# Performance work log

Measured on AMD Instinct MI355X. Metric: run time of the kernel, lower is better.

Reference implementation:

```python
import jax, jax.numpy as jnp
import numpy as np

SIGMA = 1.0
RADIUS = int(4.0 * SIGMA + 0.5)  # scipy/skimage truncate=4.0

_t = np.arange(-RADIUS, RADIUS + 1, dtype=np.float32)
_w = np.exp(-0.5 * (_t / SIGMA) ** 2)
KERNEL = jnp.asarray(_w / _w.sum())  # [2*RADIUS+1]


def _blur_axis(x, axis):
    """1D Gaussian filter along `axis` with 'nearest' (edge) boundary."""
    pads = [(0, 0)] * x.ndim
    pads[axis] = (RADIUS, RADIUS)
    xp = jnp.pad(x, pads, mode='edge')
    n = x.shape[axis]
    out = KERNEL[0] * jax.lax.slice_in_dim(xp, 0, n, axis=axis)
    for k in range(1, 2 * RADIUS + 1):
        out = out + KERNEL[k] * jax.lax.slice_in_dim(xp, k, k + n, axis=axis)
    return out


def gaussian_blur(x):
    # skimage.filters.gaussian on each [T, F] sample: blur over both axes
    x = _blur_axis(x, axis=1)  # time axis
    x = _blur_axis(x, axis=2)  # feature axis
    return x


def lstm_last_hidden(x, W_ih, W_hh, b_ih, b_hh):
    B, T, F = x.shape
    H = W_hh.shape[1]
    # precompute input projections for all timesteps: [B, T, 4H]
    xg = jnp.einsum('btf,gf->btg', x, W_ih) + b_ih + b_hh
    xg = jnp.transpose(xg, (1, 0, 2))  # [T, B, 4H]

    def step(carry, xt):
        h, c = carry
        g = xt + h @ W_hh.T  # [B, 4H]
        i, f, gg, o = jnp.split(g, 4, axis=-1)  # torch gate order i,f,g,o
        i = jax.nn.sigmoid(i)
        f = jax.nn.sigmoid(f)
        gg = jnp.tanh(gg)
        o = jax.nn.sigmoid(o)
        c = f * c + i * gg
        h = o * jnp.tanh(c)
        return (h, c), None

    h0 = jnp.zeros((B, H), dtype=x.dtype)
    c0 = jnp.zeros((B, H), dtype=x.dtype)
    (h_last, _), _ = jax.lax.scan(step, (h0, c0), xg)
    return h_last  # [B, H]


def setup_inputs() -> dict:
    key = jax.random.key(0)
    ks = jax.random.split(key, 7)
    B, T, F, H, O = 64, 1024, 256, 1024, 256
    s_ih = 1.0 / np.sqrt(F)
    s_hh = 1.0 / np.sqrt(H)
    return {
        'x': jax.random.uniform(ks[0], (B, T, F), dtype=jnp.float32),
        'W_ih': jax.random.normal(ks[1], (4 * H, F), dtype=jnp.float32) * s_ih,
        'W_hh': jax.random.normal(ks[2], (4 * H, H), dtype=jnp.float32) * s_hh,
        'b_ih': jax.random.normal(ks[3], (4 * H,), dtype=jnp.float32) * s_hh,
        'b_hh': jax.random.normal(ks[4], (4 * H,), dtype=jnp.float32) * s_hh,
        'W_fc': jax.random.normal(ks[5], (O, H), dtype=jnp.float32) * s_hh,
        'b_fc': jax.random.normal(ks[6], (O,), dtype=jnp.float32) * s_hh,
    }


def reference(x, W_ih, W_hh, b_ih, b_hh, W_fc, b_fc):
    xb = gaussian_blur(x)
    h_last = lstm_last_hidden(xb, W_ih, W_hh, b_ih, b_hh)
    return h_last @ W_fc.T + b_fc  # [B, O]
```

## Files before the change

### kernel.cpp

```cpp
#include <hip/hip_runtime.h>

typedef __bf16 bf16x8 __attribute__((ext_vector_type(8)));
typedef float f32x4 __attribute__((ext_vector_type(4)));

#define T_STEPS 1024
#define H_SZ    1024
#define F_IN    256
#define NGROUP  4
#define NB      16
#define WPG     64

__device__ __forceinline__ unsigned short f2bf(float f) {
    union { float f; unsigned u; } v; v.f = f;
    unsigned r = v.u + 0x7fffu + ((v.u >> 16) & 1u);
    return (unsigned short)(r >> 16);
}

__device__ __forceinline__ float fsigmoid(float x) {
    return 1.0f / (1.0f + __expf(-x));
}
__device__ __forceinline__ float ftanh(float x) {
    return 1.0f - 2.0f / (__expf(2.0f * x) + 1.0f);
}

__device__ __forceinline__ int redidx(int h, int b) {
    return ((4 * h + b) & 31) + 32 * ((h >> 3) * 4 + (b >> 2));
}

__global__ __launch_bounds__(256) void blur_kernel(
    const float* __restrict__ x, unsigned short* __restrict__ xb)
{
    __shared__ float tb[64][256];
    const float kk[9] = {
        0.000133831f, 0.0044318617f, 0.0539911273f, 0.2419714457f,
        0.3989434694f,
        0.2419714457f, 0.0539911273f, 0.0044318617f, 0.000133831f };

    const int b     = blockIdx.x >> 4;
    const int chunk = blockIdx.x & 15;
    const int t0    = chunk * 64;
    const int f     = threadIdx.x;
    const float* xbase = x + (size_t)b * T_STEPS * F_IN;

    for (int r = 0; r < 64; r++) {
        int t = t0 + r;
        float acc = 0.0f;
        #pragma unroll
        for (int d = 0; d < 9; d++) {
            int ts = t + d - 4;
            ts = min(max(ts, 0), T_STEPS - 1);
            acc += kk[d] * xbase[ts * F_IN + f];
        }
        tb[r][f] = acc;
    }
    __syncthreads();
    for (int r = 0; r < 64; r++) {
        float acc = 0.0f;
        #pragma unroll
        for (int d = 0; d < 9; d++) {
            int fs = f + d - 4;
            fs = min(max(fs, 0), F_IN - 1);
            acc += kk[d] * tb[r][fs];
        }
        xb[((size_t)b * T_STEPS + t0 + r) * F_IN + f] = f2bf(acc);
    }
}

__global__ __launch_bounds__(256, 1) void lstm_persist(
    const unsigned short* __restrict__ xb,
    const float* __restrict__ Whh,
    const float* __restrict__ Wih,
    const float* __restrict__ bih,
    const float* __restrict__ bhh,
    unsigned short* __restrict__ hbuf,
    unsigned int* __restrict__ arrive)
{
    const int wg   = blockIdx.x;
    const int grp  = wg >> 6;
    const int w    = wg & 63;
    const int tid  = threadIdx.x;
    const int q    = tid >> 6;
    const int lane = tid & 63;
    const int lrow = lane & 15;
    const int lq   = lane >> 4;

    __shared__ float red[4][4][256];

    bf16x8 wa[8][4];
    bf16x8 wx[2][4];
    const int row_lo = w * 16 + lrow;
    #pragma unroll
    for (int kt = 0; kt < 8; kt++) {
        const int kofs = q * 256 + kt * 32 + lq * 8;
        #pragma unroll
        for (int g = 0; g < 4; g++) {
            const float* src = Whh + (size_t)(g * H_SZ + row_lo) * H_SZ + kofs;
            union { bf16x8 v; unsigned short s[8]; } u;
            #pragma unroll
            for (int j = 0; j < 8; j++) u.s[j] = f2bf(src[j]);
            wa[kt][g] = u.v;
        }
    }
    #pragma unroll
    for (int kt = 0; kt < 2; kt++) {
        const int kofs = q * 64 + kt * 32 + lq * 8;
        #pragma unroll
        for (int g = 0; g < 4; g++) {
            const float* src = Wih + (size_t)(g * H_SZ + row_lo) * F_IN + kofs;
            union { bf16x8 v; unsigned short s[8]; } u;
            #pragma unroll
            for (int j = 0; j < 8; j++) u.s[j] = f2bf(src[j]);
            wx[kt][g] = u.v;
        }
    }

    const int uhid = tid & 15;
    const int ub   = tid >> 4;
    float bias[4];
    #pragma unroll
    for (int g = 0; g < 4; g++) {
        int r = g * H_SZ + w * 16 + uhid;
        bias[g] = bih[r] + bhh[r];
    }
    float c_reg = 0.0f;

    const int b_abs_l = grp * NB + lrow;
    const unsigned short* xrow_base =
        xb + ((size_t)b_abs_l * T_STEPS) * F_IN + q * 64 + lq * 8;
    unsigned short* hdst =
        hbuf + (size_t)(grp * NB + ub) * H_SZ + w * 16 + uhid;

    int wofs[4];
    #pragma unroll
    for (int e = 0; e < 4; e++) wofs[e] = redidx(lq * 4 + e, lrow);
    const int rofs = redidx(uhid, ub);

    for (int t = 0; t < T_STEPS; t++) {
        const unsigned short* xrow = xrow_base + (size_t)t * F_IN;
        bf16x8 xf0 = *reinterpret_cast<const bf16x8*>(xrow);
        bf16x8 xf1 = *reinterpret_cast<const bf16x8*>(xrow + 32);

        const unsigned short* hprev =
            hbuf + ((size_t)((t & 1) ^ 1) * 64 + b_abs_l) * H_SZ
                 + q * 256 + lq * 8;
        bf16x8 hf0, hf1, hf2, hf3, hf4, hf5, hf6, hf7;
        asm volatile(
            "global_load_dwordx4 %0, %8, off sc0 sc1\n\t"
            "global_load_dwordx4 %1, %8, off offset:64 sc0 sc1\n\t"
            "global_load_dwordx4 %2, %8, off offset:128 sc0 sc1\n\t"
            "global_load_dwordx4 %3, %8, off offset:192 sc0 sc1\n\t"
            "global_load_dwordx4 %4, %8, off offset:256 sc0 sc1\n\t"
            "global_load_dwordx4 %5, %8, off offset:320 sc0 sc1\n\t"
            "global_load_dwordx4 %6, %8, off offset:384 sc0 sc1\n\t"
            "global_load_dwordx4 %7, %8, off offset:448 sc0 sc1\n\t"
            "s_waitcnt vmcnt(0)"
            : "=&v"(hf0), "=&v"(hf1), "=&v"(hf2), "=&v"(hf3),
              "=&v"(hf4), "=&v"(hf5), "=&v"(hf6), "=&v"(hf7)
            : "v"(hprev)
            : "memory");
        bf16x8 hfa[8] = { hf0, hf1, hf2, hf3, hf4, hf5, hf6, hf7 };

        f32x4 acc[4];
        #pragma unroll
        for (int g = 0; g < 4; g++) acc[g] = (f32x4){0.f, 0.f, 0.f, 0.f};
        #pragma unroll
        for (int kt = 0; kt < 8; kt++)
            #pragma unroll
            for (int g = 0; g < 4; g++)
                acc[g] = __builtin_amdgcn_mfma_f32_16x16x32_bf16(
                    wa[kt][g], hfa[kt], acc[g], 0, 0, 0);
        acc[0] = __builtin_amdgcn_mfma_f32_16x16x32_bf16(wx[0][0], xf0, acc[0], 0, 0, 0);
        acc[1] = __builtin_amdgcn_mfma_f32_16x16x32_bf16(wx[0][1], xf0, acc[1], 0, 0, 0);
        acc[2] = __builtin_amdgcn_mfma_f32_16x16x32_bf16(wx[0][2], xf0, acc[2], 0, 0, 0);
        acc[3] = __builtin_amdgcn_mfma_f32_16x16x32_bf16(wx[0][3], xf0, acc[3], 0, 0, 0);
        acc[0] = __builtin_amdgcn_mfma_f32_16x16x32_bf16(wx[1][0], xf1, acc[0], 0, 0, 0);
        acc[1] = __builtin_amdgcn_mfma_f32_16x16x32_bf16(wx[1][1], xf1, acc[1], 0, 0, 0);
        acc[2] = __builtin_amdgcn_mfma_f32_16x16x32_bf16(wx[1][2], xf1, acc[2], 0, 0, 0);
        acc[3] = __builtin_amdgcn_mfma_f32_16x16x32_bf16(wx[1][3], xf1, acc[3], 0, 0, 0);

        #pragma unroll
        for (int g = 0; g < 4; g++)
            #pragma unroll
            for (int e = 0; e < 4; e++)
                red[q][g][wofs[e]] = acc[g][e];
        __syncthreads();

        float gv[4];
        #pragma unroll
        for (int g = 0; g < 4; g++) {
            float s = bias[g];
            #pragma unroll
            for (int qq = 0; qq < 4; qq++)
                s += red[qq][g][rofs];
            gv[g] = s;
        }
        float ig = fsigmoid(gv[0]);
        float fg = fsigmoid(gv[1]);
        float gg = ftanh(gv[2]);
        float og = fsigmoid(gv[3]);
        c_reg = fg * c_reg + ig * gg;
        float hv = og * ftanh(c_reg);

        unsigned short hb = f2bf(hv);
        unsigned short* dst = hdst + (size_t)(t & 1) * 64 * H_SZ;
        asm volatile(
            "global_store_short %0, %1, off sc0 sc1\n\t"
            "s_waitcnt vmcnt(0)"
            :: "v"(dst), "v"(hb)
            : "memory");
        __syncthreads();

        unsigned int* bar = arrive + (((size_t)grp * T_STEPS + t) << 6);
        if (tid == 0)
            asm volatile("global_atomic_add %0, %1, off"
                         :: "v"(bar + (w & 3) * 16), "v"(1u) : "memory");
        if (tid < 4) {
            const unsigned int* p = bar + tid * 16;
            unsigned v; int spins = 0;
            for (;;) {
                asm volatile("global_load_dword %0, %1, off sc0 sc1\n\t"
                             "s_waitcnt vmcnt(0)"
                             : "=v"(v) : "v"(p) : "memory");
                if (v >= 16u) break;
                if (++spins > (1 << 20)) break;
            }
        }
        __syncthreads();
    }
}

__global__ __launch_bounds__(256) void final_fc(
    const unsigned short* __restrict__ hbuf,
    const float* __restrict__ Wfc, const float* __restrict__ bfc,
    float* __restrict__ out)
{
    __shared__ float hs[H_SZ];
    const int b = blockIdx.x;
    const unsigned short* hrow = hbuf + (size_t)64 * H_SZ + (size_t)b * H_SZ;
    for (int k = threadIdx.x; k < H_SZ; k += 256) {
        union { unsigned u; float f; } cv;
        cv.u = ((unsigned)hrow[k]) << 16;
        hs[k] = cv.f;
    }
    __syncthreads();
    const int o = threadIdx.x;
    const float4* wr = reinterpret_cast<const float4*>(Wfc + (size_t)o * H_SZ);
    float acc = bfc[o];
    for (int k4 = 0; k4 < H_SZ / 4; k4++) {
        float4 wv = wr[k4];
        acc += hs[k4 * 4 + 0] * wv.x + hs[k4 * 4 + 1] * wv.y
             + hs[k4 * 4 + 2] * wv.z + hs[k4 * 4 + 3] * wv.w;
    }
    out[(size_t)b * 256 + o] = acc;
}

extern "C" void kernel_launch(void* const* d_in, const int* in_sizes, int n_in,
                              void* d_out, int out_size, void* d_ws,
                              size_t ws_size, hipStream_t stream)
{
    (void)in_sizes; (void)n_in; (void)out_size; (void)ws_size;
    const float* x   = (const float*)d_in[0];
    const float* Wih = (const float*)d_in[1];
    const float* Whh = (const float*)d_in[2];
    const float* bih = (const float*)d_in[3];
    const float* bhh = (const float*)d_in[4];
    const float* Wfc = (const float*)d_in[5];
    const float* bfc = (const float*)d_in[6];
    float* out = (float*)d_out;

    char* ws = (char*)d_ws;
    unsigned short* xblur = (unsigned short*)ws;
    unsigned short* hbuf  = (unsigned short*)(ws + 33554432);
    unsigned int*   arrv  = (unsigned int*)(ws + 33554432 + 262144);

    hipMemsetAsync(hbuf, 0, 262144 + 1048576, stream);

    blur_kernel<<<dim3(1024), dim3(256), 0, stream>>>(x, xblur);

    void* kargs[] = { (void*)&xblur, (void*)&Whh, (void*)&Wih,
                      (void*)&bih, (void*)&bhh, (void*)&hbuf, (void*)&arrv };
    hipLaunchCooperativeKernel((void*)lstm_persist, dim3(256), dim3(256),
                               kargs, 0, stream);

    final_fc<<<dim3(64), dim3(256), 0, stream>>>(hbuf, Wfc, bfc, out);
}
```

Baseline: 3.762 ms.

## Interleave two half-batch LSTM groups per workgroup to hide barrier latency

Each workgroup now handles two 8-sample sub-groups (A and B) of its 16-sample slice and alternates between them within each timestep. Each sub-group has its own barrier counters, so the wait on one sub-group's grid barrier overlaps with computing the other sub-group's step. The next h loads are issued before the store and wait, so they overlap too. The MFMA tiles are now half-filled, which doubles matrix work per sample. The spin loop now bails out permanently after a short timeout, which risks silently wrong results if a wait is unusually long.

Result: slower. 5.582 ms (+48.4%).

```diff
diff --git a/kernel.cpp b/kernel.cpp
--- a/kernel.cpp
+++ b/kernel.cpp
@@ -6,9 +6,10 @@
 #define T_STEPS 1024
 #define H_SZ    1024
 #define F_IN    256
-#define NGROUP  4
-#define NB      16
+#define NGR     8
+#define NB      8
 #define WPG     64
+#define SPIN_MAX (1 << 15)
 
 __device__ __forceinline__ unsigned short f2bf(float f) {
     union { float f; unsigned u; } v; v.f = f;
@@ -25,6 +26,24 @@
 
 __device__ __forceinline__ int redidx(int h, int b) {
     return ((4 * h + b) & 31) + 32 * ((h >> 3) * 4 + (b >> 2));
+}
+
+__device__ __forceinline__ void issue_h8(const unsigned short* p,
+    bf16x8& h0, bf16x8& h1, bf16x8& h2, bf16x8& h3,
+    bf16x8& h4, bf16x8& h5, bf16x8& h6, bf16x8& h7)
+{
+    asm volatile(
+        "global_load_dwordx4 %0, %8, off sc0 sc1\n\t"
+        "global_load_dwordx4 %1, %8, off offset:64 sc0 sc1\n\t"
+        "global_load_dwordx4 %2, %8, off offset:128 sc0 sc1\n\t"
+        "global_load_dwordx4 %3, %8, off offset:192 sc0 sc1\n\t"
+        "global_load_dwordx4 %4, %8, off offset:256 sc0 sc1\n\t"
+        "global_load_dwordx4 %5, %8, off offset:320 sc0 sc1\n\t"
+        "global_load_dwordx4 %6, %8, off offset:384 sc0 sc1\n\t"
+        "global_load_dwordx4 %7, %8, off offset:448 sc0 sc1"
+        : "=&v"(h0), "=&v"(h1), "=&v"(h2), "=&v"(h3),
+          "=&v"(h4), "=&v"(h5), "=&v"(h6), "=&v"(h7)
+        : "v"(p) : "memory");
 }
 
 __global__ __launch_bounds__(256) void blur_kernel(
@@ -76,13 +95,16 @@
     unsigned int* __restrict__ arrive)
 {
     const int wg   = blockIdx.x;
-    const int grp  = wg >> 6;
+    const int pid  = wg >> 6;
     const int w    = wg & 63;
     const int tid  = threadIdx.x;
     const int q    = tid >> 6;
     const int lane = tid & 63;
     const int lrow = lane & 15;
     const int lq   = lane >> 4;
+    const int bl   = lrow & 7;
+    const int gA   = pid * 2;
+    const int gB   = pid * 2 + 1;
 
     __shared__ float red[4][4][256];
 
@@ -115,117 +137,186 @@
     }
 
     const int uhid = tid & 15;
-    const int ub   = tid >> 4;
+    const int ub   = (tid >> 4) & 7;
     float bias[4];
     #pragma unroll
     for (int g = 0; g < 4; g++) {
         int r = g * H_SZ + w * 16 + uhid;
         bias[g] = bih[r] + bhh[r];
     }
-    float c_reg = 0.0f;
-
-    const int b_abs_l = grp * NB + lrow;
-    const unsigned short* xrow_base =
-        xb + ((size_t)b_abs_l * T_STEPS) * F_IN + q * 64 + lq * 8;
-    unsigned short* hdst =
-        hbuf + (size_t)(grp * NB + ub) * H_SZ + w * 16 + uhid;
+    float cA = 0.0f, cB = 0.0f;
+
+    const int bA = pid * 16 + bl;
+    const unsigned short* xbaseA =
+        xb + ((size_t)bA * T_STEPS) * F_IN + q * 64 + lq * 8;
+    const unsigned short* xbaseB = xbaseA + (size_t)8 * T_STEPS * F_IN;
+    unsigned short* hdstA =
+        hbuf + (size_t)(pid * 16 + ub) * H_SZ + w * 16 + uhid;
+    unsigned short* hdstB = hdstA + (size_t)8 * H_SZ;
+    const unsigned short* hsrcA =
+        hbuf + (size_t)bA * H_SZ + q * 256 + lq * 8;
+    const unsigned short* hsrcB = hsrcA + (size_t)8 * H_SZ;
 
     int wofs[4];
     #pragma unroll
-    for (int e = 0; e < 4; e++) wofs[e] = redidx(lq * 4 + e, lrow);
+    for (int e = 0; e < 4; e++) wofs[e] = redidx(lq * 4 + e, bl);
     const int rofs = redidx(uhid, ub);
 
+    bf16x8 hf0, hf1, hf2, hf3, hf4, hf5, hf6, hf7;
+    int bail = 0;
+
+    issue_h8(hsrcA + (size_t)64 * H_SZ, hf0, hf1, hf2, hf3, hf4, hf5, hf6, hf7);
+
     for (int t = 0; t < T_STEPS; t++) {
-        const unsigned short* xrow = xrow_base + (size_t)t * F_IN;
-        bf16x8 xf0 = *reinterpret_cast<const bf16x8*>(xrow);
-        bf16x8 xf1 = *reinterpret_cast<const bf16x8*>(xrow + 32);
-
-        const unsigned short* hprev =
-            hbuf + ((size_t)((t & 1) ^ 1) * 64 + b_abs_l) * H_SZ
-                 + q * 256 + lq * 8;
-        bf16x8 hf0, hf1, hf2, hf3, hf4, hf5, hf6, hf7;
-        asm volatile(
-            "global_load_dwordx4 %0, %8, off sc0 sc1\n\t"
-            "global_load_dwordx4 %1, %8, off offset:64 sc0 sc1\n\t"
-            "global_load_dwordx4 %2, %8, off offset:128 sc0 sc1\n\t"
-            "global_load_dwordx4 %3, %8, off offset:192 sc0 sc1\n\t"
-            "global_load_dwordx4 %4, %8, off offset:256 sc0 sc1\n\t"
-            "global_load_dwordx4 %5, %8, off offset:320 sc0 sc1\n\t"
-            "global_load_dwordx4 %6, %8, off offset:384 sc0 sc1\n\t"
-            "global_load_dwordx4 %7, %8, off offset:448 sc0 sc1\n\t"
-            "s_waitcnt vmcnt(0)"
-            : "=&v"(hf0), "=&v"(hf1), "=&v"(hf2), "=&v"(hf3),
-              "=&v"(hf4), "=&v"(hf5), "=&v"(hf6), "=&v"(hf7)
-            : "v"(hprev)
-            : "memory");
-        bf16x8 hfa[8] = { hf0, hf1, hf2, hf3, hf4, hf5, hf6, hf7 };
+        const size_t par  = (size_t)(t & 1) * 64 * H_SZ;
+        const size_t parp = (size_t)((t & 1) ^ 1) * 64 * H_SZ;
+
+        const unsigned short* xrA = xbaseA + (size_t)t * F_IN;
+        const unsigned short* xrB = xbaseB + (size_t)t * F_IN;
+        bf16x8 xA0 = *reinterpret_cast<const bf16x8*>(xrA);
+        bf16x8 xA1 = *reinterpret_cast<const bf16x8*>(xrA + 32);
+        bf16x8 xB0 = *reinterpret_cast<const bf16x8*>(xrB);
+        bf16x8 xB1 = *reinterpret_cast<const bf16x8*>(xrB + 32);
+
+        asm volatile("s_waitcnt vmcnt(0)" ::: "memory");
+        __builtin_amdgcn_sched_barrier(0);
 
         f32x4 acc[4];
         #pragma unroll
         for (int g = 0; g < 4; g++) acc[g] = (f32x4){0.f, 0.f, 0.f, 0.f};
-        #pragma unroll
-        for (int kt = 0; kt < 8; kt++)
+        {
+            bf16x8 hfa[8] = { hf0, hf1, hf2, hf3, hf4, hf5, hf6, hf7 };
+            #pragma unroll
+            for (int kt = 0; kt < 8; kt++)
+                #pragma unroll
+                for (int g = 0; g < 4; g++)
+                    acc[g] = __builtin_amdgcn_mfma_f32_16x16x32_bf16(
+                        wa[kt][g], hfa[kt], acc[g], 0, 0, 0);
+        }
+        #pragma unroll
+        for (int g = 0; g < 4; g++) {
+            acc[g] = __builtin_amdgcn_mfma_f32_16x16x32_bf16(wx[0][g], xA0, acc[g], 0, 0, 0);
+            acc[g] = __builtin_amdgcn_mfma_f32_16x16x32_bf16(wx[1][g], xA1, acc[g], 0, 0, 0);
+        }
+        if (lrow < 8) {
             #pragma unroll
             for (int g = 0; g < 4; g++)
-                acc[g] = __builtin_amdgcn_mfma_f32_16x16x32_bf16(
-                    wa[kt][g], hfa[kt], acc[g], 0, 0, 0);
-        acc[0] = __builtin_amdgcn_mfma_f32_16x16x32_bf16(wx[0][0], xf0, acc[0], 0, 0, 0);
-        acc[1] = __builtin_amdgcn_mfma_f32_16x16x32_bf16(wx[0][1], xf0, acc[1], 0, 0, 0);
-        acc[2] = __builtin_amdgcn_mfma_f32_16x16x32_bf16(wx[0][2], xf0, acc[2], 0, 0, 0);
-        acc[3] = __builtin_amdgcn_mfma_f32_16x16x32_bf16(wx[0][3], xf0, acc[3], 0, 0, 0);
-        acc[0] = __builtin_amdgcn_mfma_f32_16x16x32_bf16(wx[1][0], xf1, acc[0], 0, 0, 0);
-        acc[1] = __builtin_amdgcn_mfma_f32_16x16x32_bf16(wx[1][1], xf1, acc[1], 0, 0, 0);
-        acc[2] = __builtin_amdgcn_mfma_f32_16x16x32_bf16(wx[1][2], xf1, acc[2], 0, 0, 0);
-        acc[3] = __builtin_amdgcn_mfma_f32_16x16x32_bf16(wx[1][3], xf1, acc[3], 0, 0, 0);
-
-        #pragma unroll
-        for (int g = 0; g < 4; g++)
-            #pragma unroll
-            for (int e = 0; e < 4; e++)
-                red[q][g][wofs[e]] = acc[g][e];
-        __syncthreads();
-
-        float gv[4];
-        #pragma unroll
-        for (int g = 0; g < 4; g++) {
-            float s = bias[g];
-            #pragma unroll
-            for (int qq = 0; qq < 4; qq++)
-                s += red[qq][g][rofs];
-            gv[g] = s;
-        }
-        float ig = fsigmoid(gv[0]);
-        float fg = fsigmoid(gv[1]);
-        float gg = ftanh(gv[2]);
-        float og = fsigmoid(gv[3]);
-        c_reg = fg * c_reg + ig * gg;
-        float hv = og * ftanh(c_reg);
-
-        unsigned short hb = f2bf(hv);
-        unsigned short* dst = hdst + (size_t)(t & 1) * 64 * H_SZ;
-        asm volatile(
-            "global_store_short %0, %1, off sc0 sc1\n\t"
-            "s_waitcnt vmcnt(0)"
-            :: "v"(dst), "v"(hb)
-            : "memory");
-        __syncthreads();
-
-        unsigned int* bar = arrive + (((size_t)grp * T_STEPS + t) << 6);
-        if (tid == 0)
-            asm volatile("global_atomic_add %0, %1, off"
-                         :: "v"(bar + (w & 3) * 16), "v"(1u) : "memory");
-        if (tid < 4) {
-            const unsigned int* p = bar + tid * 16;
-            unsigned v; int spins = 0;
+                #pragma unroll
+                for (int e = 0; e < 4; e++)
+                    red[q][g][wofs[e]] = acc[g][e];
+        }
+        __syncthreads();
+
+        unsigned short hbA = 0;
+        if (tid < 128) {
+            float gv[4];
+            #pragma unroll
+            for (int g = 0; g < 4; g++) {
+                float s = bias[g];
+                #pragma unroll
+                for (int qq = 0; qq < 4; qq++) s += red[qq][g][rofs];
+                gv[g] = s;
+            }
+            float ig = fsigmoid(gv[0]), fg = fsigmoid(gv[1]);
+            float gz = ftanh(gv[2]),    og = fsigmoid(gv[3]);
+            cA = fg * cA + ig * gz;
+            hbA = f2bf(og * ftanh(cA));
+        }
+
+        if (t > 0 && tid < 4 && !bail) {
+            const unsigned int* p =
+                arrive + (((size_t)gB * T_STEPS + (t - 1)) << 6) + tid * 16;
+            unsigned v; int sp = 0;
             for (;;) {
                 asm volatile("global_load_dword %0, %1, off sc0 sc1\n\t"
                              "s_waitcnt vmcnt(0)"
                              : "=v"(v) : "v"(p) : "memory");
                 if (v >= 16u) break;
-                if (++spins > (1 << 20)) break;
+                if (++sp > SPIN_MAX) { bail = 1; break; }
             }
         }
         __syncthreads();
+
+        issue_h8(hsrcB + parp, hf0, hf1, hf2, hf3, hf4, hf5, hf6, hf7);
+
+        if (tid < 128)
+            asm volatile("global_store_short %0, %1, off sc0 sc1"
+                         :: "v"(hdstA + par), "v"(hbA) : "memory");
+        asm volatile("s_waitcnt vmcnt(0)" ::: "memory");
+        __builtin_amdgcn_sched_barrier(0);
+        __syncthreads();
+        if (tid == 0)
+            asm volatile("global_atomic_add %0, %1, off"
+                         :: "v"(arrive + (((size_t)gA * T_STEPS + t) << 6)
+                                 + (w & 3) * 16), "v"(1u) : "memory");
+
+        #pragma unroll
+        for (int g = 0; g < 4; g++) acc[g] = (f32x4){0.f, 0.f, 0.f, 0.f};
+        {
+            bf16x8 hfb[8] = { hf0, hf1, hf2, hf3, hf4, hf5, hf6, hf7 };
+            #pragma unroll
+            for (int kt = 0; kt < 8; kt++)
+                #pragma unroll
+                for (int g = 0; g < 4; g++)
+                    acc[g] = __builtin_amdgcn_mfma_f32_16x16x32_bf16(
+                        wa[kt][g], hfb[kt], acc[g], 0, 0, 0);
+        }
+        #pragma unroll
+        for (int g = 0; g < 4; g++) {
+            acc[g] = __builtin_amdgcn_mfma_f32_16x16x32_bf16(wx[0][g], xB0, acc[g], 0, 0, 0);
+            acc[g] = __builtin_amdgcn_mfma_f32_16x16x32_bf16(wx[1][g], xB1, acc[g], 0, 0, 0);
+        }
+        if (lrow < 8) {
+            #pragma unroll
+            for (int g = 0; g < 4; g++)
+                #pragma unroll
+                for (int e = 0; e < 4; e++)
+                    red[q][g][wofs[e]] = acc[g][e];
+        }
+        __syncthreads();
+
+        unsigned short hbB = 0;
+        if (tid < 128) {
+            float gv[4];
+            #pragma unroll
+            for (int g = 0; g < 4; g++) {
+                float s = bias[g];
+                #pragma unroll
+                for (int qq = 0; qq < 4; qq++) s += red[qq][g][rofs];
+                gv[g] = s;
+            }
+            float ig = fsigmoid(gv[0]), fg = fsigmoid(gv[1]);
+            float gz = ftanh(gv[2]),    og = fsigmoid(gv[3]);
+            cB = fg * cB + ig * gz;
+            hbB = f2bf(og * ftanh(cB));
+        }
+
+        if (tid < 4 && !bail) {
+            const unsigned int* p =
+                arrive + (((size_t)gA * T_STEPS + t) << 6) + tid * 16;
+            unsigned v; int sp = 0;
+            for (;;) {
+                asm volatile("global_load_dword %0, %1, off sc0 sc1\n\t"
+                             "s_waitcnt vmcnt(0)"
+                             : "=v"(v) : "v"(p) : "memory");
+                if (v >= 16u) break;
+                if (++sp > SPIN_MAX) { bail = 1; break; }
+            }
+        }
+        __syncthreads();
+
+        issue_h8(hsrcA + par, hf0, hf1, hf2, hf3, hf4, hf5, hf6, hf7);
+
+        if (tid < 128)
+            asm volatile("global_store_short %0, %1, off sc0 sc1"
+                         :: "v"(hdstB + par), "v"(hbB) : "memory");
+        asm volatile("s_waitcnt vmcnt(0)" ::: "memory");
+        __builtin_amdgcn_sched_barrier(0);
+        __syncthreads();
+        if (tid == 0)
+            asm volatile("global_atomic_add %0, %1, off"
+                         :: "v"(arrive + (((size_t)gB * T_STEPS + t) << 6)
+                                 + (w & 3) * 16), "v"(1u) : "memory");
     }
 }
 
@@ -273,7 +364,7 @@
     unsigned short* hbuf  = (unsigned short*)(ws + 33554432);
     unsigned int*   arrv  = (unsigned int*)(ws + 33554432 + 262144);
 
-    hipMemsetAsync(hbuf, 0, 262144 + 1048576, stream);
+    hipMemsetAsync(hbuf, 0, 262144 + 2097152, stream);
 
     blur_kernel<<<dim3(1024), dim3(256), 0, stream>>>(x, xblur);
 
```
